# Kernel optimization log

Hardware: AMD Instinct MI355X
Metric: run time of the kernel (lower is better)

Reference implementation:

```python
import jax, jax.numpy as jnp
import numpy as np

B, S, D, H, HD, FFN_MULT = 4, 2048, 2048, 16, 128, 4
EPS = 1e-8


def setup_inputs() -> dict:
    key = jax.random.key(0)
    ks = jax.random.split(key, 12)
    s = lambda k, shape, scale: (jax.random.normal(k, shape, dtype=jnp.float32) * scale)
    d_ff = D * FFN_MULT
    return {
        "x": s(ks[0], (B, S, D), 1.0),
        # per-head Q/K/V projections, stacked: [H, D, HD] (no bias, as in source)
        "wq": s(ks[1], (H, D, HD), D ** -0.5),
        "wk": s(ks[2], (H, D, HD), D ** -0.5),
        "wv": s(ks[3], (H, D, HD), D ** -0.5),
        # output projection Linear(D, D) with bias
        "wo": s(ks[4], (D, D), D ** -0.5),
        "bo": jnp.zeros((D,), jnp.float32),
        # FFN: Linear(D, d_ff) -> ReLU -> Linear(d_ff, D), both with bias
        "w1": s(ks[5], (D, d_ff), D ** -0.5),
        "b1": jnp.zeros((d_ff,), jnp.float32),
        "w2": s(ks[6], (d_ff, D), d_ff ** -0.5),
        "b2": jnp.zeros((D,), jnp.float32),
        # RMSNorm gains
        "g1": jnp.ones((D,), jnp.float32),
        "g2": jnp.ones((D,), jnp.float32),
    }


def rms_norm(x, g):
    return x * jax.lax.rsqrt(jnp.mean(x * x, axis=-1, keepdims=True) + EPS) * g


def attention(h, wq, wk, wv, wo, bo):
    # per-head projections batched over heads: [B,S,D] x [H,D,K] -> [B,H,S,K]
    q = jnp.einsum("bsd,hdk->bhsk", h, wq)
    k = jnp.einsum("bsd,hdk->bhsk", h, wk)
    v = jnp.einsum("bsd,hdk->bhsk", h, wv)
    scores = jnp.einsum("bhsk,bhtk->bhst", q, k) * (HD ** -0.5)
    causal = jnp.tril(jnp.ones((S, S), dtype=bool))
    scores = jnp.where(causal, scores, -jnp.inf)
    attn = jax.nn.softmax(scores, axis=-1)
    out = jnp.einsum("bhst,bhtk->bhsk", attn, v)  # [B,H,S,HD]
    # concat heads along feature dim (head order matches torch.cat over heads)
    out = out.transpose(0, 2, 1, 3).reshape(B, S, D)
    return out @ wo + bo


def reference(x, wq, wk, wv, wo, bo, w1, b1, w2, b2, g1, g2):
    x = x + attention(rms_norm(x, g1), wq, wk, wv, wo, bo)
    h = rms_norm(x, g2)
    ffn = jax.nn.relu(h @ w1 + b1) @ w2 + b2
    return x + ffn
```

## Files before the change

kernel.cpp:

```cpp
#include <hip/hip_runtime.h>
#include <hip/hip_bf16.h>

#define Bsz 4
#define Ssz 2048
#define Dsz 2048
#define Hn 16
#define HDsz 128
#define DFF 8192
#define Msz (Bsz*Ssz)

typedef __bf16 bf16x8 __attribute__((ext_vector_type(8)));
typedef float  f32x4  __attribute__((ext_vector_type(4)));

enum { FLAG_BIAS=1, FLAG_RELU=2, FLAG_RESID=4, FLAG_F32OUT=8, FLAG_QKV=16 };

#define GLDS16(g, l) __builtin_amdgcn_global_load_lds( \
    (const __attribute__((address_space(1))) unsigned int*)(g), \
    (__attribute__((address_space(3))) unsigned int*)(l), 16, 0, 0)

template <typename TIN>
__global__ __launch_bounds__(256) void transpose_cvt(
    const TIN* __restrict__ in, __bf16* __restrict__ out,
    int R, int C, long long inRS, int subB,
    long long strideOuter, long long strideInner, long long outBS)
{
  __shared__ float tile[32][33];
  int bz = blockIdx.z;
  const TIN* inp = in + (size_t)(bz / subB) * strideOuter + (size_t)(bz % subB) * strideInner;
  __bf16* outp = out + (size_t)bz * outBS;
  int tx = threadIdx.x, ty = threadIdx.y;
  int c  = blockIdx.x * 32 + tx;
  int r0 = blockIdx.y * 32;
#pragma unroll
  for (int i = 0; i < 4; ++i) {
    int r = r0 + ty + i * 8;
    tile[ty + i * 8][tx] = (float)inp[(size_t)r * inRS + c];
  }
  __syncthreads();
  int oc  = r0 + tx;
  int or0 = blockIdx.x * 32;
#pragma unroll
  for (int i = 0; i < 4; ++i) {
    int orr = or0 + ty + i * 8;
    outp[(size_t)orr * R + oc] = (__bf16)tile[tx][ty + i * 8];
  }
}

__global__ __launch_bounds__(256) void rmsnorm_k(
    const float* __restrict__ x, const float* __restrict__ g, __bf16* __restrict__ out)
{
  int row = blockIdx.x, tid = threadIdx.x;
  const float4* xr = (const float4*)(x + (size_t)row * Dsz);
  float4 v0 = xr[tid*2], v1 = xr[tid*2+1];
  float ss = v0.x*v0.x + v0.y*v0.y + v0.z*v0.z + v0.w*v0.w
           + v1.x*v1.x + v1.y*v1.y + v1.z*v1.z + v1.w*v1.w;
#pragma unroll
  for (int off = 32; off > 0; off >>= 1) ss += __shfl_down(ss, off);
  __shared__ float wsum[4];
  __shared__ float sc;
  if ((tid & 63) == 0) wsum[tid >> 6] = ss;
  __syncthreads();
  if (tid == 0) {
    float t = wsum[0] + wsum[1] + wsum[2] + wsum[3];
    sc = rsqrtf(t * (1.0f / (float)Dsz) + 1e-8f);
  }
  __syncthreads();
  float s = sc;
  const float4* gr = (const float4*)g;
  float4 g0 = gr[tid*2], g1v = gr[tid*2+1];
  bf16x8 ov;
  ov[0]=(__bf16)(v0.x*s*g0.x);  ov[1]=(__bf16)(v0.y*s*g0.y);
  ov[2]=(__bf16)(v0.z*s*g0.z);  ov[3]=(__bf16)(v0.w*s*g0.w);
  ov[4]=(__bf16)(v1.x*s*g1v.x); ov[5]=(__bf16)(v1.y*s*g1v.y);
  ov[6]=(__bf16)(v1.z*s*g1v.z); ov[7]=(__bf16)(v1.w*s*g1v.w);
  *(bf16x8*)(out + (size_t)row * Dsz + tid * 8) = ov;
}

#define SBAR       asm volatile("s_barrier" ::: "memory")
#define WAIT_VM2   asm volatile("s_waitcnt vmcnt(2)" ::: "memory")
#define WAIT_VM0   asm volatile("s_waitcnt vmcnt(0)" ::: "memory")

#define STG1(Xb, Xlds, buf, kst) \
    GLDS16((Xb) + (size_t)rloc * K + (kst) + sloc, (Xlds) + (buf)*16384 + wuni)

#define LDA(mi) (*(const bf16x8*)(AsB + cur*16384 + (wr*64 + (mi)*16 + l15)*64 + psl))
#define LDB(nj) (*(const bf16x8*)(BsB + cur*16384 + (wc*64 + (nj)*16 + l15)*64 + psl))

__global__ __launch_bounds__(1024) void gemm256(
    const __bf16* __restrict__ A, const __bf16* __restrict__ B,
    const float* __restrict__ bias, const float* __restrict__ resid,
    void* __restrict__ Cout, void* __restrict__ CoutV,
    int M, int N, int K, int flags)
{
  __shared__ __align__(16) __bf16 As[3*256*32];
  __shared__ __align__(16) __bf16 Bs[3*256*32];
  int nwg = gridDim.x;
  int id = blockIdx.x;
  id = (id & 7) * (nwg >> 3) + (id >> 3);
  int ntn = N >> 8;
  int tm = id / ntn, tn = id - tm * ntn;
  int tid = threadIdx.x;
  int lane = tid & 63, w = tid >> 6;
  int l15 = lane & 15, lg = lane >> 4;
  int wr = w >> 2, wc = w & 3;
  const __bf16* Ab = A + (size_t)tm * 256 * K;
  const __bf16* Bb = B + (size_t)tn * 256 * K;
  char* AsB = (char*)As;
  char* BsB = (char*)Bs;
  int rloc = tid >> 2;
  int sloc = ((lane & 3) ^ ((lane >> 3) & 3)) * 8;
  int wuni = w * 1024;
  int psl  = (lg ^ ((l15 >> 1) & 3)) * 16;
  f32x4 zero; zero[0]=0.f; zero[1]=0.f; zero[2]=0.f; zero[3]=0.f;
  f32x4 acc[4][4];
#pragma unroll
  for (int i = 0; i < 4; ++i)
#pragma unroll
    for (int j = 0; j < 4; ++j) acc[i][j] = zero;
  int NT = K >> 5;
  STG1(Ab, AsB, 0, 0);
  STG1(Bb, BsB, 0, 0);
  STG1(Ab, AsB, 1, 32);
  STG1(Bb, BsB, 1, 32);
  WAIT_VM2; SBAR;
  int cur = 0;
  for (int t = 0; t < NT; ++t) {
    int sb = cur + 2; if (sb >= 3) sb -= 3;
    int kst = (t + 2 < NT) ? ((t + 2) << 5) : 0;
    STG1(Ab, AsB, sb, kst);
    STG1(Bb, BsB, sb, kst);
    bf16x8 af[4], bf[4];
    af[0]=LDA(0); af[1]=LDA(1); af[2]=LDA(2); af[3]=LDA(3);
    bf[0]=LDB(0); bf[1]=LDB(1); bf[2]=LDB(2); bf[3]=LDB(3);
#pragma unroll
    for (int mi = 0; mi < 4; ++mi)
#pragma unroll
      for (int nj = 0; nj < 4; ++nj)
        acc[mi][nj] = __builtin_amdgcn_mfma_f32_16x16x32_bf16(af[mi], bf[nj], acc[mi][nj], 0, 0, 0);
    WAIT_VM2;
    SBAR;
    cur += 1; if (cur >= 3) cur -= 3;
  }
  WAIT_VM0;
  int cm = tm * 256 + wr * 64;
  int cn = tn * 256 + wc * 64;
  float*  Cf = (float*)Cout;
  __bf16* Cb;
  int Ns = N, cnb = cn;
  if (flags & FLAG_QKV) {
    int which = cn >> 11;
    Cb = (which == 2) ? (__bf16*)CoutV
                      : ((__bf16*)Cout + (size_t)which * Msz * 2048);
    Ns = 2048; cnb = cn & 2047;
  } else {
    Cb = (__bf16*)Cout;
  }
#pragma unroll
  for (int m = 0; m < 4; ++m) {
#pragma unroll
    for (int nj = 0; nj < 4; ++nj) {
      int col  = cn  + nj * 16 + l15;
      int colo = cnb + nj * 16 + l15;
      float bv = (flags & FLAG_BIAS) ? bias[col] : 0.0f;
#pragma unroll
      for (int r = 0; r < 4; ++r) {
        int row = cm + m * 16 + 4 * lg + r;
        float v = acc[m][nj][r] + bv;
        if (flags & FLAG_RELU) v = v > 0.f ? v : 0.f;
        size_t idx = (size_t)row * Ns + colo;
        if (flags & FLAG_RESID) v += resid[idx];
        if (flags & FLAG_F32OUT) Cf[idx] = v;
        else                     Cb[idx] = (__bf16)v;
      }
    }
  }
}

__global__ __launch_bounds__(512) void fattn(
    const __bf16* __restrict__ q, const __bf16* __restrict__ k,
    const __bf16* __restrict__ vt, __bf16* __restrict__ o)
{
  __shared__ __align__(16) __bf16 Ks[64*128];
  __shared__ __align__(16) __bf16 Vs[128*64];
  __shared__ __align__(16) __bf16 Ps[8][16*72];
  int bx = blockIdx.x, bh = blockIdx.y;
  int b = bh >> 4, h = bh & 15;
  int tid = threadIdx.x, lane = tid & 63, w = tid >> 6;
  int l15 = lane & 15, lg = lane >> 4;
  size_t base = ((size_t)b * Ssz) * Dsz + (size_t)h * HDsz;
  size_t vtb  = (size_t)bh * HDsz * Ssz;
  const float scale = 0.08838834764831845f;
  char* KsB = (char*)Ks;
  char* VsB = (char*)Vs;
  f32x4 zero; zero[0]=0.f; zero[1]=0.f; zero[2]=0.f; zero[3]=0.f;

  for (int ph = 0; ph < 2; ++ph) {
    int qt = ph ? bx : (15 - bx);
    int qs = qt * 128;
    int qmin = qs + w * 16;
    bf16x8 qf[4];
    int qrow = qmin + l15;
#pragma unroll
    for (int kk = 0; kk < 4; ++kk)
      qf[kk] = *(const bf16x8*)(q + base + (size_t)qrow * Dsz + kk * 32 + lg * 8);
    f32x4 acc[8];
#pragma unroll
    for (int i = 0; i < 8; ++i) acc[i] = zero;
    float mr[4], lr[4];
#pragma unroll
    for (int r = 0; r < 4; ++r) { mr[r] = -1e30f; lr[r] = 0.f; }
    int NT = 2 * qt + 2;
    for (int kt = 0; kt < NT; ++kt) {
      int t0 = kt * 64;
#pragma unroll
      for (int j = 0; j < 2; ++j) {
        int c = tid + j * 512;
        int tr = c >> 4, hc = c & 15;
        bf16x8 tk = *(const bf16x8*)(k + base + (size_t)(t0 + tr) * Dsz + hc * 8);
        *(bf16x8*)(KsB + ((tr * 256 + hc * 16) ^ ((tr & 7) << 4))) = tk;
        int hd = c >> 3, tc = c & 7;
        bf16x8 tv = *(const bf16x8*)(vt + vtb + (size_t)hd * Ssz + t0 + tc * 8);
        *(bf16x8*)(VsB + ((hd * 128 + tc * 16) ^ ((hd & 7) << 4))) = tv;
      }
      __syncthreads();
      bool act = (t0 <= qmin + 15);
      if (act) {
        f32x4 s[4];
#pragma unroll
        for (int cg = 0; cg < 4; ++cg) s[cg] = zero;
        __builtin_amdgcn_s_setprio(1);
#pragma unroll
        for (int kk = 0; kk < 4; ++kk) {
#pragma unroll
          for (int cg = 0; cg < 4; ++cg) {
            int tl = cg * 16 + l15;
            bf16x8 kf = *(const bf16x8*)(KsB + ((tl * 256 + kk * 64 + lg * 16) ^ ((tl & 7) << 4)));
            s[cg] = __builtin_amdgcn_mfma_f32_16x16x32_bf16(qf[kk], kf, s[cg], 0, 0, 0);
          }
        }
        __builtin_amdgcn_s_setprio(0);
        bool nm = (t0 + 63 > qmin);
        float rm[4];
        bool sk = true;
#pragma unroll
        for (int r = 0; r < 4; ++r) {
          int qr = qmin + 4 * lg + r;
          float m0 = -1e30f;
#pragma unroll
          for (int cg = 0; cg < 4; ++cg) {
            float sv = s[cg][r] * scale;
            if (nm && (t0 + cg * 16 + l15) > qr) sv = -1e30f;
            s[cg][r] = sv;
            m0 = fmaxf(m0, sv);
          }
          m0 = fmaxf(m0, __shfl_xor(m0, 1));
          m0 = fmaxf(m0, __shfl_xor(m0, 2));
          m0 = fmaxf(m0, __shfl_xor(m0, 4));
          m0 = fmaxf(m0, __shfl_xor(m0, 8));
          rm[r] = m0;
          sk = sk && (m0 <= mr[r] + 8.0f);
        }
        if (!__all(sk)) {
          f32x4 av;
#pragma unroll
          for (int r = 0; r < 4; ++r) {
            float mn = fmaxf(mr[r], rm[r]);
            float a = __expf(mr[r] - mn);
            mr[r] = mn;
            lr[r] *= a;
            av[r] = a;
          }
#pragma unroll
          for (int hg = 0; hg < 8; ++hg) acc[hg] *= av;
        }
#pragma unroll
        for (int r = 0; r < 4; ++r) {
          float ps = 0.f;
#pragma unroll
          for (int cg = 0; cg < 4; ++cg) {
            float p = __expf(s[cg][r] - mr[r]);
            Ps[w][(4 * lg + r) * 72 + cg * 16 + l15] = (__bf16)p;
            ps += p;
          }
          ps += __shfl_xor(ps, 1);
          ps += __shfl_xor(ps, 2);
          ps += __shfl_xor(ps, 4);
          ps += __shfl_xor(ps, 8);
          lr[r] += ps;
        }
        __builtin_amdgcn_s_setprio(1);
#pragma unroll
        for (int tt = 0; tt < 2; ++tt) {
          bf16x8 pf = *(const bf16x8*)((char*)&Ps[w][0] + l15 * 144 + tt * 64 + lg * 16);
#pragma unroll
          for (int hg = 0; hg < 8; ++hg) {
            int hd = hg * 16 + l15;
            bf16x8 vf = *(const bf16x8*)(VsB + ((hd * 128 + tt * 64 + lg * 16) ^ ((hd & 7) << 4)));
            acc[hg] = __builtin_amdgcn_mfma_f32_16x16x32_bf16(pf, vf, acc[hg], 0, 0, 0);
          }
        }
        __builtin_amdgcn_s_setprio(0);
      }
      __syncthreads();
    }
    f32x4 inv;
#pragma unroll
    for (int r = 0; r < 4; ++r) inv[r] = 1.0f / lr[r];
#pragma unroll
    for (int hg = 0; hg < 8; ++hg) {
      f32x4 ov = acc[hg] * inv;
#pragma unroll
      for (int r = 0; r < 4; ++r) {
        int qr2 = qmin + 4 * lg + r;
        o[base + (size_t)qr2 * Dsz + hg * 16 + l15] = (__bf16)ov[r];
      }
    }
  }
}

extern "C" void kernel_launch(void* const* d_in, const int* in_sizes, int n_in,
                              void* d_out, int out_size, void* d_ws, size_t ws_size,
                              hipStream_t stream)
{
  (void)in_sizes; (void)n_in; (void)out_size; (void)ws_size;
  const float* x  = (const float*)d_in[0];
  const float* wq = (const float*)d_in[1];
  const float* wk = (const float*)d_in[2];
  const float* wv = (const float*)d_in[3];
  const float* wo = (const float*)d_in[4];
  const float* bo = (const float*)d_in[5];
  const float* w1 = (const float*)d_in[6];
  const float* b1 = (const float*)d_in[7];
  const float* w2 = (const float*)d_in[8];
  const float* b2 = (const float*)d_in[9];
  const float* g1 = (const float*)d_in[10];
  const float* g2 = (const float*)d_in[11];
  float* out = (float*)d_out;
  char* ws = (char*)d_ws;

  const size_t U = (size_t)2048 * 2048 * 2;
  __bf16* wqT = (__bf16*)(ws);
  __bf16* wkT = (__bf16*)(ws + U);
  __bf16* wvT = (__bf16*)(ws + 2*U);
  __bf16* woT = (__bf16*)(ws + 3*U);
  __bf16* w1T = (__bf16*)(ws + 4*U);
  __bf16* w2T = (__bf16*)(ws + 8*U);
  __bf16* h1  = (__bf16*)(ws + 12*U);
  __bf16* vb  = (__bf16*)(ws + 16*U);
  __bf16* vT    = h1;
  __bf16* attno = vb;
  __bf16* fb    = h1;
  __bf16* h2    = (__bf16*)(ws);
  __bf16* qb = (__bf16*)d_out;
  __bf16* kb = qb + (size_t)Msz * Dsz;
  float*  x2 = (float*)d_out;

  dim3 tb(32, 8, 1);
  transpose_cvt<float><<<dim3(4,64,16),  tb, 0, stream>>>(wq, wqT, 2048, 128, 128, 1, (long long)2048*128, 0, (long long)128*2048);
  transpose_cvt<float><<<dim3(4,64,16),  tb, 0, stream>>>(wk, wkT, 2048, 128, 128, 1, (long long)2048*128, 0, (long long)128*2048);
  transpose_cvt<float><<<dim3(4,64,16),  tb, 0, stream>>>(wv, wvT, 2048, 128, 128, 1, (long long)2048*128, 0, (long long)128*2048);
  transpose_cvt<float><<<dim3(64,64,1),  tb, 0, stream>>>(wo, woT, 2048, 2048, 2048, 1, 0, 0, 0);
  transpose_cvt<float><<<dim3(256,64,1), tb, 0, stream>>>(w1, w1T, 2048, 8192, 8192, 1, 0, 0, 0);
  transpose_cvt<float><<<dim3(64,128,2), tb, 0, stream>>>(w2, w2T, 4096, 2048, 2048, 1, (long long)4096*2048, 0, (long long)2048*4096);
  rmsnorm_k<<<8192, 256, 0, stream>>>(x, g1, h1);
  gemm256<<<768, 1024, 0, stream>>>(h1, wqT, nullptr, nullptr, qb, vb, Msz, 6144, 2048, FLAG_QKV);
  transpose_cvt<__bf16><<<dim3(4,64,64), tb, 0, stream>>>(vb, vT, 2048, 128, 2048, 16, (long long)2048*2048, 128, (long long)128*2048);
  fattn<<<dim3(8, 64), 512, 0, stream>>>(qb, kb, vT, attno);
  gemm256<<<256, 1024, 0, stream>>>(attno, woT, bo, x, x2, nullptr, Msz, 2048, 2048, FLAG_BIAS | FLAG_RESID | FLAG_F32OUT);
  rmsnorm_k<<<8192, 256, 0, stream>>>(x2, g2, h2);
  for (int c = 0; c < 2; ++c) {
    gemm256<<<512, 1024, 0, stream>>>(h2, w1T + (size_t)c*4096*2048, b1 + c*4096, nullptr,
                                      fb, nullptr, Msz, 4096, 2048, FLAG_BIAS | FLAG_RELU);
    int fl = FLAG_RESID | FLAG_F32OUT | (c == 0 ? FLAG_BIAS : 0);
    gemm256<<<256, 1024, 0, stream>>>(fb, w2T + (size_t)c*2048*4096, b2, x2,
                                      out, nullptr, Msz, 2048, 4096, fl);
  }
}
```

Baseline: 1.318 ms.

## Switch GEMM main loop to double-buffered 64-wide K steps

Replaces the 3-stage, 32-wide-K LDS ring in the 256x256 GEMM with a 2-stage double buffer that loads 64 K-elements per iteration as two 32-wide halves. This halves the number of barriers and loop iterations per K and doubles the compute between synchronisations. In exchange, prefetch depth drops from two stages to one and each iteration waits for all outstanding loads (vmcnt 0), so load latency may be less well hidden. LDS use rises from 96KB to 128KB per block.

```diff
diff --git a/kernel.cpp b/kernel.cpp
--- a/kernel.cpp
+++ b/kernel.cpp
@@ -77,14 +77,13 @@
 }
 
 #define SBAR       asm volatile("s_barrier" ::: "memory")
-#define WAIT_VM2   asm volatile("s_waitcnt vmcnt(2)" ::: "memory")
 #define WAIT_VM0   asm volatile("s_waitcnt vmcnt(0)" ::: "memory")
 
-#define STG1(Xb, Xlds, buf, kst) \
-    GLDS16((Xb) + (size_t)rloc * K + (kst) + sloc, (Xlds) + (buf)*16384 + wuni)
-
-#define LDA(mi) (*(const bf16x8*)(AsB + cur*16384 + (wr*64 + (mi)*16 + l15)*64 + psl))
-#define LDB(nj) (*(const bf16x8*)(BsB + cur*16384 + (wc*64 + (nj)*16 + l15)*64 + psl))
+#define STG2(Xb, Xlds, buf, kh, kst) \
+    GLDS16((Xb) + (size_t)rloc * K + (kst) + (kh)*32 + sloc, (Xlds) + (buf)*32768 + (kh)*16384 + wuni)
+
+#define LDA2(kh, mi) (*(const bf16x8*)(AsB + cur*32768 + (kh)*16384 + (wr*64 + (mi)*16 + l15)*64 + psl))
+#define LDB2(kh, nj) (*(const bf16x8*)(BsB + cur*32768 + (kh)*16384 + (wc*64 + (nj)*16 + l15)*64 + psl))
 
 __global__ __launch_bounds__(1024) void gemm256(
     const __bf16* __restrict__ A, const __bf16* __restrict__ B,
@@ -92,8 +91,8 @@
     void* __restrict__ Cout, void* __restrict__ CoutV,
     int M, int N, int K, int flags)
 {
-  __shared__ __align__(16) __bf16 As[3*256*32];
-  __shared__ __align__(16) __bf16 Bs[3*256*32];
+  __shared__ __align__(16) __bf16 As[2*2*256*32];
+  __shared__ __align__(16) __bf16 Bs[2*2*256*32];
   int nwg = gridDim.x;
   int id = blockIdx.x;
   id = (id & 7) * (nwg >> 3) + (id >> 3);
@@ -117,31 +116,44 @@
   for (int i = 0; i < 4; ++i)
 #pragma unroll
     for (int j = 0; j < 4; ++j) acc[i][j] = zero;
-  int NT = K >> 5;
-  STG1(Ab, AsB, 0, 0);
-  STG1(Bb, BsB, 0, 0);
-  STG1(Ab, AsB, 1, 32);
-  STG1(Bb, BsB, 1, 32);
-  WAIT_VM2; SBAR;
+  int NT = K >> 6;
+  STG2(Ab, AsB, 0, 0, 0);
+  STG2(Ab, AsB, 0, 1, 0);
+  STG2(Bb, BsB, 0, 0, 0);
+  STG2(Bb, BsB, 0, 1, 0);
+  WAIT_VM0; SBAR;
   int cur = 0;
   for (int t = 0; t < NT; ++t) {
-    int sb = cur + 2; if (sb >= 3) sb -= 3;
-    int kst = (t + 2 < NT) ? ((t + 2) << 5) : 0;
-    STG1(Ab, AsB, sb, kst);
-    STG1(Bb, BsB, sb, kst);
-    bf16x8 af[4], bf[4];
-    af[0]=LDA(0); af[1]=LDA(1); af[2]=LDA(2); af[3]=LDA(3);
-    bf[0]=LDB(0); bf[1]=LDB(1); bf[2]=LDB(2); bf[3]=LDB(3);
-#pragma unroll
-    for (int mi = 0; mi < 4; ++mi)
-#pragma unroll
-      for (int nj = 0; nj < 4; ++nj)
-        acc[mi][nj] = __builtin_amdgcn_mfma_f32_16x16x32_bf16(af[mi], bf[nj], acc[mi][nj], 0, 0, 0);
-    WAIT_VM2;
+    int nb = cur ^ 1;
+    int kst = (t + 1 < NT) ? ((t + 1) << 6) : 0;
+    STG2(Ab, AsB, nb, 0, kst);
+    STG2(Ab, AsB, nb, 1, kst);
+    STG2(Bb, BsB, nb, 0, kst);
+    STG2(Bb, BsB, nb, 1, kst);
+    {
+      bf16x8 af[4], bf[4];
+      af[0]=LDA2(0,0); af[1]=LDA2(0,1); af[2]=LDA2(0,2); af[3]=LDA2(0,3);
+      bf[0]=LDB2(0,0); bf[1]=LDB2(0,1); bf[2]=LDB2(0,2); bf[3]=LDB2(0,3);
+#pragma unroll
+      for (int mi = 0; mi < 4; ++mi)
+#pragma unroll
+        for (int nj = 0; nj < 4; ++nj)
+          acc[mi][nj] = __builtin_amdgcn_mfma_f32_16x16x32_bf16(af[mi], bf[nj], acc[mi][nj], 0, 0, 0);
+    }
+    {
+      bf16x8 af[4], bf[4];
+      af[0]=LDA2(1,0); af[1]=LDA2(1,1); af[2]=LDA2(1,2); af[3]=LDA2(1,3);
+      bf[0]=LDB2(1,0); bf[1]=LDB2(1,1); bf[2]=LDB2(1,2); bf[3]=LDB2(1,3);
+#pragma unroll
+      for (int mi = 0; mi < 4; ++mi)
+#pragma unroll
+        for (int nj = 0; nj < 4; ++nj)
+          acc[mi][nj] = __builtin_amdgcn_mfma_f32_16x16x32_bf16(af[mi], bf[nj], acc[mi][nj], 0, 0, 0);
+    }
+    WAIT_VM0;
     SBAR;
-    cur += 1; if (cur >= 3) cur -= 3;
-  }
-  WAIT_VM0;
+    cur = nb;
+  }
   int cm = tm * 256 + wr * 64;
   int cn = tn * 256 + wc * 64;
   float*  Cf = (float*)Cout;
```

Result: no change. 1.335 ms (+1.3%).
